# Kernel tuning notes

Hardware: AMD Instinct MI355X
Metric: run time of the kernel (lower is better)

## Reference

```python
import jax, jax.numpy as jnp
import numpy as np

BS, C, H, W = 64, 3, 512, 512
DROP_PIX = 0.3          # fraction of pixels dropped
NOISE_STD = 0.1         # gaussian multiplicative noise std
RNG_SEED = 42           # internal forward randomness (torch RNG analog)


def setup_inputs() -> dict:
    key = jax.random.key(0)
    x = jax.random.normal(key, (BS, C, H, W), dtype=jnp.float32)
    return {"x": x}


def reference(x):
    bs, c, h, w = x.shape
    hw = h * w
    len_keep = int(hw * (1.0 - DROP_PIX))
    k_mask, k_noise = jax.random.split(jax.random.key(RNG_SEED))

    # Per-sample random permutation of pixel indices, keep first len_keep.
    # argsort of iid uniforms == uniformly random permutation (all bs at once,
    # replacing the Python loop + per-iteration randperm of the original).
    u = jax.random.uniform(k_mask, (bs, hw))
    keep_idx = jnp.argsort(u, axis=1)[:, :len_keep]          # [bs, len_keep]
    mask = jnp.zeros((bs, hw), dtype=x.dtype)
    mask = mask.at[jnp.arange(bs)[:, None], keep_idx].set(1.0)
    mask = mask.reshape(bs, 1, h, w)

    # drop_type == 'zeros'
    x = x * mask

    # additive_noise: gaussian multiplicative noise (real-valued branch)
    noise = jax.random.normal(k_noise, x.shape, dtype=x.dtype) * NOISE_STD + 1.0
    x = x * noise
    return x, mask
```

## Files before the change

### kernel.cpp

```cpp
#include <hip/hip_runtime.h>
#include <hip/hip_bf16.h>

typedef unsigned int u32;
typedef unsigned long long u64;

__host__ __device__ __forceinline__ void tf2x32(u32 k0, u32 k1, u32 x0, u32 x1,
                                                u32& o0, u32& o1)
{
    const u32 ks2 = k0 ^ k1 ^ 0x1BD11BDAu;
    x0 += k0; x1 += k1;
#define TF_R(r) { x0 += x1; x1 = (x1 << (r)) | (x1 >> (32 - (r))); x1 ^= x0; }
    TF_R(13) TF_R(15) TF_R(26) TF_R(6)
    x0 += k1; x1 += ks2 + 1u;
    TF_R(17) TF_R(29) TF_R(16) TF_R(24)
    x0 += ks2; x1 += k0 + 2u;
    TF_R(13) TF_R(15) TF_R(26) TF_R(6)
    x0 += k0; x1 += k1 + 3u;
    TF_R(17) TF_R(29) TF_R(16) TF_R(24)
    x0 += k1; x1 += ks2 + 4u;
    TF_R(13) TF_R(15) TF_R(26) TF_R(6)
    x0 += ks2; x1 += k0 + 5u;
#undef TF_R
    o0 = x0; o1 = x1;
}

__device__ __forceinline__ u32 rbits(u32 k0, u32 k1, u32 e)
{
    u32 o0, o1; tf2x32(k0, k1, 0u, e, o0, o1); return o0 ^ o1;
}

#define HW        262144u
#define PMASK     262143u
#define KEEP      183500u
#define NX        50331648u
#define NM        16777216u
#define LO_F      (-0.99999994039535522461f)

__device__ __forceinline__ float noise_from_bits(u32 bits)
{
    float f  = __uint_as_float((bits >> 9) | 0x3F800000u) - 1.0f;
    float un = fmaf(f, 2.0f, LO_F);
    un = fmaxf(LO_F, un);
    float w = -__logf(fmaf(-un, un, 1.0f));
    float p;
    if (w < 5.0f) {
        w -= 2.5f;
        p = 2.81022636e-08f;
        p = fmaf(p, w, 3.43273939e-07f);
        p = fmaf(p, w, -3.5233877e-06f);
        p = fmaf(p, w, -4.39150654e-06f);
        p = fmaf(p, w, 0.00021858087f);
        p = fmaf(p, w, -0.00125372503f);
        p = fmaf(p, w, -0.00417768164f);
        p = fmaf(p, w, 0.246640727f);
        p = fmaf(p, w, 1.50140941f);
    } else {
        w = __fsqrt_rn(w) - 3.0f;
        p = -0.000200214257f;
        p = fmaf(p, w, 0.000100950558f);
        p = fmaf(p, w, 0.00134934322f);
        p = fmaf(p, w, -0.00367342844f);
        p = fmaf(p, w, 0.00573950773f);
        p = fmaf(p, w, -0.0076224613f);
        p = fmaf(p, w, 0.00943887047f);
        p = fmaf(p, w, 1.00167406f);
        p = fmaf(p, w, 2.83297682f);
    }
    float ei = p * un;
    return fmaf(1.41421356f * ei, 0.1f, 1.0f);
}

__global__ __launch_bounds__(256) void k1_gen(u32 mk0, u32 mk1, uint4* mv)
{
    u32 tid = blockIdx.x * 256u + threadIdx.x;
    u32 e = tid << 2;
    uint4 q;
    q.x = rbits(mk0, mk1, e)      >> 9;
    q.y = rbits(mk0, mk1, e + 1u) >> 9;
    q.z = rbits(mk0, mk1, e + 2u) >> 9;
    q.w = rbits(mk0, mk1, e + 3u) >> 9;
    mv[tid] = q;
}

__global__ __launch_bounds__(1024) void k2_select(const u32* mbuf, u64* rowsel)
{
    __shared__ u32 hist[4096];
    __shared__ u32 sh[1026];
    __shared__ u32 cand[512];
    __shared__ u32 ccnt;
    const int t = threadIdx.x;
    const u32 row = blockIdx.x;
    const uint4* mv = (const uint4*)mbuf + ((u64)row << 16);

    for (int i = t; i < 4096; i += 1024) hist[i] = 0;
    if (t == 0) ccnt = 0;
    __syncthreads();

#pragma unroll 1
    for (int i = 0; i < 64; ++i) {
        uint4 q = mv[(i << 10) + t];
        atomicAdd(&hist[q.x >> 11], 1u);
        atomicAdd(&hist[q.y >> 11], 1u);
        atomicAdd(&hist[q.z >> 11], 1u);
        atomicAdd(&hist[q.w >> 11], 1u);
    }
    __syncthreads();

    u32 v0 = hist[t * 4], v1 = hist[t * 4 + 1], v2 = hist[t * 4 + 2], v3 = hist[t * 4 + 3];
    sh[t] = v0 + v1 + v2 + v3;
    __syncthreads();
    if (t == 0) {
        u32 run = 0, c = 0;
        for (; c < 1023u; ++c) { u32 cs = sh[c]; if (run + cs >= KEEP) break; run += cs; }
        sh[1024] = c; sh[1025] = run;
    }
    __syncthreads();
    u32 c = sh[1024];
    if (t == (int)c) {
        u32 run = sh[1025];
        u32 v[4] = { v0, v1, v2, v3 };
        u32 b = (u32)t * 4u + 3u, r = KEEP - run;
#pragma unroll
        for (int i = 0; i < 4; ++i) {
            if (run + v[i] >= KEEP) { b = (u32)t * 4u + (u32)i; r = KEEP - run; break; }
            run += v[i];
        }
        sh[1024] = b; sh[1025] = r;
    }
    __syncthreads();
    const u32 B = sh[1024];
    const u32 r = sh[1025];
    __syncthreads();

#pragma unroll 1
    for (int i = 0; i < 64; ++i) {
        u32 vi = (u32)(i << 10) + (u32)t;
        uint4 q = mv[vi];
        u32 p = vi << 2;
        if ((q.x >> 11) == B) { u32 pos = atomicAdd(&ccnt, 1u); if (pos < 512u) cand[pos] = ((q.x & 2047u) << 18) | p; }
        if ((q.y >> 11) == B) { u32 pos = atomicAdd(&ccnt, 1u); if (pos < 512u) cand[pos] = ((q.y & 2047u) << 18) | (p + 1u); }
        if ((q.z >> 11) == B) { u32 pos = atomicAdd(&ccnt, 1u); if (pos < 512u) cand[pos] = ((q.z & 2047u) << 18) | (p + 2u); }
        if ((q.w >> 11) == B) { u32 pos = atomicAdd(&ccnt, 1u); if (pos < 512u) cand[pos] = ((q.w & 2047u) << 18) | (p + 3u); }
    }
    __syncthreads();

    u32 cnt = ccnt; if (cnt > 512u) cnt = 512u;
    if ((u32)t < cnt) {
        u32 me = cand[t];
        u32 rk = 0;
        for (u32 j = 0; j < cnt; ++j) rk += (cand[j] < me) ? 1u : 0u;
        if (rk == r - 1u) {
            u32 mstar = (B << 11) | (me >> 18);
            rowsel[row] = ((u64)mstar << 18) | (u64)(me & 0x3FFFFu);
        }
    }
}

__global__ __launch_bounds__(256) void k3_fused(const float4* x4, u32* mmask,
                                                const u64* rowsel, float4* out4,
                                                u32 nk0, u32 nk1)
{
    u32 tid = blockIdx.x * 256u + threadIdx.x;
    u32 b  = tid >> 16;
    u32 pq = tid & 65535u;
    u32 p  = pq << 2;
    u64 kst = rowsel[b];
    uint4 q = ((const uint4*)mmask)[tid];
    float4 mk;
    mk.x = ((((u64)q.x << 18) | (u64)p)        <= kst) ? 1.0f : 0.0f;
    mk.y = ((((u64)q.y << 18) | (u64)(p + 1u)) <= kst) ? 1.0f : 0.0f;
    mk.z = ((((u64)q.z << 18) | (u64)(p + 2u)) <= kst) ? 1.0f : 0.0f;
    mk.w = ((((u64)q.w << 18) | (u64)(p + 3u)) <= kst) ? 1.0f : 0.0f;
#pragma unroll
    for (u32 ch = 0; ch < 3u; ++ch) {
        u32 xi = ((b * 3u + ch) << 16) + pq;
        u32 e  = ((b * 3u + ch) << 18) + p;
        float4 xv = x4[xi];
        float4 rr;
        rr.x = (xv.x * mk.x) * noise_from_bits(rbits(nk0, nk1, e));
        rr.y = (xv.y * mk.y) * noise_from_bits(rbits(nk0, nk1, e + 1u));
        rr.z = (xv.z * mk.z) * noise_from_bits(rbits(nk0, nk1, e + 2u));
        rr.w = (xv.w * mk.w) * noise_from_bits(rbits(nk0, nk1, e + 3u));
        out4[xi] = rr;
    }
    ((float4*)mmask)[tid] = mk;
}

extern "C" void kernel_launch(void* const* d_in, const int* in_sizes, int n_in,
                              void* d_out, int out_size, void* d_ws, size_t ws_size,
                              hipStream_t stream) {
    const float* x = (const float*)d_in[0];
    float* xout = (float*)d_out;
    u32*  mmask = (u32*)(xout + NX);
    u64*  rowsel = (u64*)d_ws;

    u32 mk0, mk1, nk0, nk1;
    tf2x32(0u, 42u, 0u, 0u, mk0, mk1);
    tf2x32(0u, 42u, 0u, 1u, nk0, nk1);

    k1_gen<<<16384, 256, 0, stream>>>(mk0, mk1, (uint4*)mmask);
    k2_select<<<64, 1024, 0, stream>>>(mmask, rowsel);
    k3_fused<<<16384, 256, 0, stream>>>((const float4*)x, mmask, rowsel,
                                        (float4*)xout, nk0, nk1);
    (void)d_ws; (void)ws_size; (void)in_sizes; (void)n_in; (void)out_size;
}
```

Before: 527.0 us.

## Replace materialized mask bits with windowed histogram, candidate select, and recomputation

Stops writing the per-pixel random keys to memory and reading them back twice. A parallel histogram kernel regenerates the keys, counts the elements below a fixed window of bins near the expected keep threshold, and collects candidates that fall inside that window. A small select kernel then finds the exact threshold key from those candidates, falling back to a full per-row recomputation if the window misses. The fused output kernel regenerates the mask keys instead of loading them. This trades memory traffic and the 64-block serial selection for extra Threefry computation and global atomics.

```diff
diff --git a/kernel.cpp b/kernel.cpp
--- a/kernel.cpp
+++ b/kernel.cpp
@@ -30,10 +30,13 @@
 }
 
 #define HW        262144u
-#define PMASK     262143u
 #define KEEP      183500u
 #define NX        50331648u
 #define NM        16777216u
+#define WLO       2835u
+#define NWIN      65u
+#define CAP       8192u
+#define LCAP      1024u
 #define LO_F      (-0.99999994039535522461f)
 
 __device__ __forceinline__ float noise_from_bits(u32 bits)
@@ -70,107 +73,140 @@
     return fmaf(1.41421356f * ei, 0.1f, 1.0f);
 }
 
-__global__ __launch_bounds__(256) void k1_gen(u32 mk0, u32 mk1, uint4* mv)
-{
-    u32 tid = blockIdx.x * 256u + threadIdx.x;
-    u32 e = tid << 2;
-    uint4 q;
-    q.x = rbits(mk0, mk1, e)      >> 9;
-    q.y = rbits(mk0, mk1, e + 1u) >> 9;
-    q.z = rbits(mk0, mk1, e + 2u) >> 9;
-    q.w = rbits(mk0, mk1, e + 3u) >> 9;
-    mv[tid] = q;
-}
-
-__global__ __launch_bounds__(1024) void k2_select(const u32* mbuf, u64* rowsel)
-{
-    __shared__ u32 hist[4096];
-    __shared__ u32 sh[1026];
-    __shared__ u32 cand[512];
-    __shared__ u32 ccnt;
+__global__ __launch_bounds__(256) void kA_hist(u32 mk0, u32 mk1, u32* winhist,
+                                               u32* candcnt, u64* cand)
+{
+    __shared__ u32 wh[NWIN];
+    __shared__ u32 red[256];
+    const int t = threadIdx.x;
+    const u32 blk = blockIdx.x;
+    const u32 row = blk >> 4;
+    const u32 base = blk << 14;
+    for (int i = t; i < (int)NWIN; i += 256) wh[i] = 0;
+    __syncthreads();
+    u32 below = 0;
+#pragma unroll 1
+    for (int i = 0; i < 16; ++i) {
+        u32 vi = (u32)(i << 8) + (u32)t;
+        u32 e = base + (vi << 2);
+        u32 p = e & (HW - 1u);
+        u32 m0 = rbits(mk0, mk1, e)      >> 9;
+        u32 m1 = rbits(mk0, mk1, e + 1u) >> 9;
+        u32 m2 = rbits(mk0, mk1, e + 2u) >> 9;
+        u32 m3 = rbits(mk0, mk1, e + 3u) >> 9;
+#define DO_EL(mm, pp) { u32 bin = (mm) >> 11; below += (bin < WLO) ? 1u : 0u;          \
+        u32 wb = bin - WLO;                                                            \
+        if (wb < NWIN) { atomicAdd(&wh[wb], 1u);                                       \
+            u32 pos = atomicAdd(&candcnt[row], 1u);                                    \
+            if (pos < CAP) cand[((u64)row << 13) + pos] = ((u64)(mm) << 18) | (u64)(pp); } }
+        DO_EL(m0, p) DO_EL(m1, p + 1u) DO_EL(m2, p + 2u) DO_EL(m3, p + 3u)
+#undef DO_EL
+    }
+    red[t] = below;
+    __syncthreads();
+    for (int s = 128; s > 0; s >>= 1) { if (t < s) red[t] += red[t + s]; __syncthreads(); }
+    if (t == 0 && red[0]) atomicAdd(&winhist[row * 66u], red[0]);
+    if (t < (int)NWIN) { u32 v = wh[t]; if (v) atomicAdd(&winhist[row * 66u + 1u + (u32)t], v); }
+}
+
+__global__ __launch_bounds__(256) void kB_select(u32 mk0, u32 mk1,
+                                                 const u32* winhist, const u32* candcnt,
+                                                 const u64* cand, u64* rowsel)
+{
+    __shared__ u64 lc[LCAP];
+    __shared__ u32 fh[4096];
+    __shared__ u32 lcnt, sB, sr, sfb;
     const int t = threadIdx.x;
     const u32 row = blockIdx.x;
-    const uint4* mv = (const uint4*)mbuf + ((u64)row << 16);
-
-    for (int i = t; i < 4096; i += 1024) hist[i] = 0;
-    if (t == 0) ccnt = 0;
-    __syncthreads();
-
-#pragma unroll 1
-    for (int i = 0; i < 64; ++i) {
-        uint4 q = mv[(i << 10) + t];
-        atomicAdd(&hist[q.x >> 11], 1u);
-        atomicAdd(&hist[q.y >> 11], 1u);
-        atomicAdd(&hist[q.z >> 11], 1u);
-        atomicAdd(&hist[q.w >> 11], 1u);
-    }
-    __syncthreads();
-
-    u32 v0 = hist[t * 4], v1 = hist[t * 4 + 1], v2 = hist[t * 4 + 2], v3 = hist[t * 4 + 3];
-    sh[t] = v0 + v1 + v2 + v3;
-    __syncthreads();
     if (t == 0) {
-        u32 run = 0, c = 0;
-        for (; c < 1023u; ++c) { u32 cs = sh[c]; if (run + cs >= KEEP) break; run += cs; }
-        sh[1024] = c; sh[1025] = run;
-    }
-    __syncthreads();
-    u32 c = sh[1024];
-    if (t == (int)c) {
-        u32 run = sh[1025];
-        u32 v[4] = { v0, v1, v2, v3 };
-        u32 b = (u32)t * 4u + 3u, r = KEEP - run;
+        u32 bl = winhist[row * 66u];
+        u32 cum = bl, B = 0xFFFFFFFFu, r = 0;
+        if (KEEP > bl) {
+            for (u32 i = 0; i < NWIN; ++i) {
+                u32 h = winhist[row * 66u + 1u + i];
+                if (cum + h >= KEEP) { B = WLO + i; r = KEEP - cum; break; }
+                cum += h;
+            }
+        }
+        sfb = (B == 0xFFFFFFFFu || candcnt[row] > CAP) ? 1u : 0u;
+        sB = B; sr = r; lcnt = 0;
+    }
+    __syncthreads();
+    if (sfb) {
+        for (int i = t; i < 4096; i += 256) fh[i] = 0;
+        __syncthreads();
+        for (u32 i = (u32)t; i < 65536u; i += 256u) {
+            u32 e = (row << 18) + (i << 2);
+            u32 m0 = rbits(mk0, mk1, e) >> 9, m1 = rbits(mk0, mk1, e + 1u) >> 9;
+            u32 m2 = rbits(mk0, mk1, e + 2u) >> 9, m3 = rbits(mk0, mk1, e + 3u) >> 9;
+            atomicAdd(&fh[m0 >> 11], 1u); atomicAdd(&fh[m1 >> 11], 1u);
+            atomicAdd(&fh[m2 >> 11], 1u); atomicAdd(&fh[m3 >> 11], 1u);
+        }
+        __syncthreads();
+        if (t == 0) {
+            u32 cum = 0;
+            for (u32 i = 0; i < 4096u; ++i) {
+                u32 h = fh[i];
+                if (cum + h >= KEEP) { sB = i; sr = KEEP - cum; break; }
+                cum += h;
+            }
+        }
+        __syncthreads();
+        for (u32 i = (u32)t; i < 65536u; i += 256u) {
+            u32 e = (row << 18) + (i << 2);
+            u32 p = i << 2;
+            u32 mm[4];
+            mm[0] = rbits(mk0, mk1, e) >> 9; mm[1] = rbits(mk0, mk1, e + 1u) >> 9;
+            mm[2] = rbits(mk0, mk1, e + 2u) >> 9; mm[3] = rbits(mk0, mk1, e + 3u) >> 9;
 #pragma unroll
-        for (int i = 0; i < 4; ++i) {
-            if (run + v[i] >= KEEP) { b = (u32)t * 4u + (u32)i; r = KEEP - run; break; }
-            run += v[i];
-        }
-        sh[1024] = b; sh[1025] = r;
-    }
-    __syncthreads();
-    const u32 B = sh[1024];
-    const u32 r = sh[1025];
-    __syncthreads();
-
-#pragma unroll 1
-    for (int i = 0; i < 64; ++i) {
-        u32 vi = (u32)(i << 10) + (u32)t;
-        uint4 q = mv[vi];
-        u32 p = vi << 2;
-        if ((q.x >> 11) == B) { u32 pos = atomicAdd(&ccnt, 1u); if (pos < 512u) cand[pos] = ((q.x & 2047u) << 18) | p; }
-        if ((q.y >> 11) == B) { u32 pos = atomicAdd(&ccnt, 1u); if (pos < 512u) cand[pos] = ((q.y & 2047u) << 18) | (p + 1u); }
-        if ((q.z >> 11) == B) { u32 pos = atomicAdd(&ccnt, 1u); if (pos < 512u) cand[pos] = ((q.z & 2047u) << 18) | (p + 2u); }
-        if ((q.w >> 11) == B) { u32 pos = atomicAdd(&ccnt, 1u); if (pos < 512u) cand[pos] = ((q.w & 2047u) << 18) | (p + 3u); }
-    }
-    __syncthreads();
-
-    u32 cnt = ccnt; if (cnt > 512u) cnt = 512u;
-    if ((u32)t < cnt) {
-        u32 me = cand[t];
+            for (u32 j = 0; j < 4u; ++j)
+                if ((mm[j] >> 11) == sB) {
+                    u32 pos = atomicAdd(&lcnt, 1u);
+                    if (pos < LCAP) lc[pos] = ((u64)mm[j] << 18) | (u64)(p + j);
+                }
+        }
+    } else {
+        u32 cnt = candcnt[row];
+        for (u32 i = (u32)t; i < cnt; i += 256u) {
+            u64 k = cand[((u64)row << 13) + i];
+            if ((u32)(k >> 29) == sB) {
+                u32 pos = atomicAdd(&lcnt, 1u);
+                if (pos < LCAP) lc[pos] = k;
+            }
+        }
+    }
+    __syncthreads();
+    u32 n = lcnt; if (n > LCAP) n = LCAP;
+    u32 want = sr - 1u;
+    for (u32 i = (u32)t; i < n; i += 256u) {
+        u64 me = lc[i];
         u32 rk = 0;
-        for (u32 j = 0; j < cnt; ++j) rk += (cand[j] < me) ? 1u : 0u;
-        if (rk == r - 1u) {
-            u32 mstar = (B << 11) | (me >> 18);
-            rowsel[row] = ((u64)mstar << 18) | (u64)(me & 0x3FFFFu);
-        }
-    }
-}
-
-__global__ __launch_bounds__(256) void k3_fused(const float4* x4, u32* mmask,
-                                                const u64* rowsel, float4* out4,
-                                                u32 nk0, u32 nk1)
+        for (u32 j = 0; j < n; ++j) rk += (lc[j] < me) ? 1u : 0u;
+        if (rk == want) rowsel[row] = me;
+    }
+}
+
+__global__ __launch_bounds__(256) void kC_fused(const float4* __restrict__ x4,
+                                                float4* __restrict__ out4,
+                                                float4* __restrict__ maskout,
+                                                const u64* __restrict__ rowsel,
+                                                u32 mk0, u32 mk1, u32 nk0, u32 nk1)
 {
     u32 tid = blockIdx.x * 256u + threadIdx.x;
     u32 b  = tid >> 16;
     u32 pq = tid & 65535u;
     u32 p  = pq << 2;
     u64 kst = rowsel[b];
-    uint4 q = ((const uint4*)mmask)[tid];
+    u32 em = (b << 18) + p;
+    u32 q0 = rbits(mk0, mk1, em)      >> 9;
+    u32 q1 = rbits(mk0, mk1, em + 1u) >> 9;
+    u32 q2 = rbits(mk0, mk1, em + 2u) >> 9;
+    u32 q3 = rbits(mk0, mk1, em + 3u) >> 9;
     float4 mk;
-    mk.x = ((((u64)q.x << 18) | (u64)p)        <= kst) ? 1.0f : 0.0f;
-    mk.y = ((((u64)q.y << 18) | (u64)(p + 1u)) <= kst) ? 1.0f : 0.0f;
-    mk.z = ((((u64)q.z << 18) | (u64)(p + 2u)) <= kst) ? 1.0f : 0.0f;
-    mk.w = ((((u64)q.w << 18) | (u64)(p + 3u)) <= kst) ? 1.0f : 0.0f;
+    mk.x = ((((u64)q0 << 18) | (u64)p)        <= kst) ? 1.0f : 0.0f;
+    mk.y = ((((u64)q1 << 18) | (u64)(p + 1u)) <= kst) ? 1.0f : 0.0f;
+    mk.z = ((((u64)q2 << 18) | (u64)(p + 2u)) <= kst) ? 1.0f : 0.0f;
+    mk.w = ((((u64)q3 << 18) | (u64)(p + 3u)) <= kst) ? 1.0f : 0.0f;
 #pragma unroll
     for (u32 ch = 0; ch < 3u; ++ch) {
         u32 xi = ((b * 3u + ch) << 16) + pq;
@@ -183,7 +219,7 @@
         rr.w = (xv.w * mk.w) * noise_from_bits(rbits(nk0, nk1, e + 3u));
         out4[xi] = rr;
     }
-    ((float4*)mmask)[tid] = mk;
+    maskout[tid] = mk;
 }
 
 extern "C" void kernel_launch(void* const* d_in, const int* in_sizes, int n_in,
@@ -191,16 +227,22 @@
                               hipStream_t stream) {
     const float* x = (const float*)d_in[0];
     float* xout = (float*)d_out;
-    u32*  mmask = (u32*)(xout + NX);
-    u64*  rowsel = (u64*)d_ws;
+    float* maskout = xout + NX;
+
+    u32* wsu = (u32*)d_ws;
+    u32* winhist = wsu;
+    u32* candcnt = wsu + 4224;
+    u64* cand    = (u64*)(wsu + 8192);
+    u64* rowsel  = (u64*)(wsu + 8192u + 64u * 8192u * 2u);
 
     u32 mk0, mk1, nk0, nk1;
     tf2x32(0u, 42u, 0u, 0u, mk0, mk1);
     tf2x32(0u, 42u, 0u, 1u, nk0, nk1);
 
-    k1_gen<<<16384, 256, 0, stream>>>(mk0, mk1, (uint4*)mmask);
-    k2_select<<<64, 1024, 0, stream>>>(mmask, rowsel);
-    k3_fused<<<16384, 256, 0, stream>>>((const float4*)x, mmask, rowsel,
-                                        (float4*)xout, nk0, nk1);
-    (void)d_ws; (void)ws_size; (void)in_sizes; (void)n_in; (void)out_size;
-}
+    hipMemsetAsync(wsu, 0, (4224u + 64u) * sizeof(u32), stream);
+    kA_hist<<<1024, 256, 0, stream>>>(mk0, mk1, winhist, candcnt, cand);
+    kB_select<<<64, 256, 0, stream>>>(mk0, mk1, winhist, candcnt, cand, rowsel);
+    kC_fused<<<16384, 256, 0, stream>>>((const float4*)x, (float4*)xout,
+                                        (float4*)maskout, rowsel, mk0, mk1, nk0, nk1);
+    (void)ws_size; (void)in_sizes; (void)n_in; (void)out_size;
+}
```

Result: slower. 1.243 ms (+135.9%).
